# Performance work log

Hardware: AMD Instinct MI355X
Metric: run time of the kernel (lower is better)

The kernel has to match this reference:

```python
import jax, jax.numpy as jnp
import numpy as np

NEG_INF = -9e15
ALPHA = 0.2  # attention leaky_relu slope


def _gat_layer(h, adj_mask, W, a1, a2):
    # h: [N, Fin], W: [Fin, D], a1/a2: [D]
    Wh = h @ W                                   # [N, D]
    f1 = Wh @ a1                                 # [N]
    f2 = Wh @ a2                                 # [N]
    e = jax.nn.leaky_relu(f1[:, None] + f2[None, :], ALPHA)  # [N, N]
    scores = jnp.where(adj_mask, e, NEG_INF)
    att = jax.nn.softmax(scores, axis=-1)        # row-normalized over neighbors
    return att @ Wh                              # [N, D]


def setup_inputs() -> dict:
    key = jax.random.key(0)
    ks = jax.random.split(key, 12)
    N, Fin, H, D, C = 4096, 512, 8, 64, 64
    s = 0.1
    x = jax.random.normal(ks[0], (N, Fin), jnp.float32)
    adj = jax.random.randint(ks[1], (N, N), 0, 2, jnp.int32)
    W = jax.random.normal(ks[2], (H, Fin, D), jnp.float32) * s
    a1 = jax.random.normal(ks[3], (H, D), jnp.float32) * s
    a2 = jax.random.normal(ks[4], (H, D), jnp.float32) * s
    Wo = jax.random.normal(ks[5], (H * D, C), jnp.float32) * s
    ao1 = jax.random.normal(ks[6], (C,), jnp.float32) * s
    ao2 = jax.random.normal(ks[7], (C,), jnp.float32) * s
    W1 = jax.random.normal(ks[8], (512, N), jnp.float32) * 0.01  # nn.Linear(N, 512)
    b1 = jnp.zeros((512,), jnp.float32)
    W2 = jax.random.normal(ks[9], (256, 512), jnp.float32) * 0.04  # nn.Linear(512, 256)
    b2 = jnp.zeros((256,), jnp.float32)
    return {"x": x, "adj": adj, "W": W, "a1": a1, "a2": a2,
            "Wo": Wo, "ao1": ao1, "ao2": ao2,
            "W1": W1, "b1": b1, "W2": W2, "b2": b2}


def reference(x, adj, W, a1, a2, Wo, ao1, ao2, W1, b1, W2, b2):
    mask = adj > 0                                    # [N, N]
    # multi-head dense attention, concat=True -> ELU per head
    heads = jax.vmap(lambda Wk, a1k, a2k: _gat_layer(x, mask, Wk, a1k, a2k))(W, a1, a2)  # [H, N, D]
    h = jax.nn.elu(heads).transpose(1, 0, 2).reshape(x.shape[0], -1)  # [N, H*D]
    # output attention layer, concat=False (no inner ELU), then outer ELU
    out = jax.nn.elu(_gat_layer(h, mask, Wo, ao1, ao2))  # [N, C]
    out = jax.nn.log_softmax(out, axis=0)                # over nodes (dim=0)
    # MLP head on transposed features: [C, N] -> [C, 512] -> [C, 256]
    y = jax.nn.leaky_relu(out.T @ W1.T + b1, 0.1)
    y = y @ W2.T + b2
    return y
```

## Files before the change

### kernel.cpp

```cpp
#include <hip/hip_runtime.h>
#include <hip/hip_bf16.h>
#include <math.h>


#define N_NODES 4096
#define FIN 512
#define NHEAD 8
#define DHEAD 64
#define NCLS 64

typedef unsigned short u16;
typedef unsigned long long u64;
typedef __attribute__((ext_vector_type(8))) short bf16x8;
typedef __attribute__((ext_vector_type(4))) float f32x4;

__device__ __forceinline__ float lrelu02(float x) { return x > 0.f ? x : 0.2f * x; }
__device__ __forceinline__ u16 bf16u(float x) {
    __hip_bfloat16 h = __float2bfloat16(x);
    return __builtin_bit_cast(unsigned short, h);
}
__device__ __forceinline__ f32x4 mfma16(bf16x8 a, bf16x8 b, f32x4 c) {
    return __builtin_amdgcn_mfma_f32_16x16x32_bf16(a, b, c, 0, 0, 0);
}
__device__ __forceinline__ unsigned fkey(float f) {
    unsigned u = __builtin_bit_cast(unsigned, f);
    return (u & 0x80000000u) ? ~u : (u | 0x80000000u);
}
__device__ __forceinline__ float funkey(unsigned k) {
    unsigned u = (k & 0x80000000u) ? (k ^ 0x80000000u) : ~k;
    return __builtin_bit_cast(float, u);
}

__global__ __launch_bounds__(256) void prep(
    const int* __restrict__ adj, u64* __restrict__ mbT, unsigned* __restrict__ gmk,
    const float* __restrict__ x, u16* __restrict__ xB,
    const float* __restrict__ W1, u16* __restrict__ W1B,
    const float* __restrict__ W, const float* __restrict__ Wo,
    u16* __restrict__ WBt, u16* __restrict__ WoBt) {
    __shared__ alignas(16) u16 T[64][72];
    const int bid = blockIdx.x, t = threadIdx.x;
    if (bid < 1024) {
        if (bid == 0 && t < 16) gmk[t] = 0u;
        int nwaves = (1024 * 256) >> 6;
        int wid = (bid * 256 + t) >> 6;
        int lane = t & 63;
        for (int w = wid; w < N_NODES * 64; w += nwaves) {
            int i = w >> 6, wc = w & 63;
            int j = (wc << 6) | lane;
            u64 m = __ballot(adj[(size_t)i * N_NODES + j] > 0);
            if (lane == 0) mbT[(size_t)wc * N_NODES + i] = m;
        }
    } else if (bid < 5120) {
        int i = (bid - 1024) * 256 + t;
        const float* s;
        u16* d;
        if (i < N_NODES * FIN / 4) { s = x; d = xB; }
        else { i -= N_NODES * FIN / 4; s = W1; d = W1B; }
        float4 v = ((const float4*)s)[i];
        ushort4 o = {bf16u(v.x), bf16u(v.y), bf16u(v.z), bf16u(v.w)};
        ((ushort4*)d)[i] = o;
    } else {
        int idx = bid - 5120;
        int y = idx >> 3, xb = idx & 7;
        const float* src = (y < 8) ? W + (size_t)y * FIN * DHEAD : Wo;
        u16* d = (y < 8) ? WBt + (size_t)y * DHEAD * FIN : WoBt;
        const int j0 = xb * 64;
        const int row = t & 63, g = t >> 6;
        #pragma unroll
        for (int k = 0; k < 16; k += 4) {
            float4 v = *(const float4*)(src + (size_t)(j0 + row) * 64 + g * 16 + k);
            T[g * 16 + k + 0][row] = bf16u(v.x);
            T[g * 16 + k + 1][row] = bf16u(v.y);
            T[g * 16 + k + 2][row] = bf16u(v.z);
            T[g * 16 + k + 3][row] = bf16u(v.w);
        }
        __syncthreads();
        const int dd = t >> 2, jc = (t & 3) * 16;
        *(uint4*)(d + (size_t)dd * FIN + j0 + jc) = *(const uint4*)&T[dd][jc];
        *(uint4*)(d + (size_t)dd * FIN + j0 + jc + 8) = *(const uint4*)&T[dd][jc + 8];
    }
}

__global__ __launch_bounds__(256) void gemm_fused(
    const u16* __restrict__ A, int lda, const u16* __restrict__ Bt, int ldb,
    const float* __restrict__ a1a, const float* __restrict__ a2a,
    u16* __restrict__ WhBT, float* __restrict__ f1o, float* __restrict__ f2o,
    unsigned* __restrict__ gmk, int K) {
    __shared__ alignas(16) u16 T[64][72];
    const int t = threadIdx.x, lane = t & 63, wv = t >> 6;
    const int c16 = lane & 15, kg = lane >> 4;
    const int h = blockIdx.x;
    const int bm = blockIdx.y * 64;
    const u16* Ap = A + (size_t)(bm + wv * 16 + c16) * lda + kg * 8;
    const u16* Bp = Bt + (size_t)(h * 64 + c16) * ldb + kg * 8;
    f32x4 acc[4] = {};
    #pragma unroll 4
    for (int k0 = 0; k0 < K; k0 += 32) {
        bf16x8 a = *(const bf16x8*)(Ap + k0);
        #pragma unroll
        for (int ct = 0; ct < 4; ++ct) {
            bf16x8 b = *(const bf16x8*)(Bp + (size_t)ct * 16 * ldb + k0);
            acc[ct] = mfma16(a, b, acc[ct]);
        }
    }
    float a1v[4], a2v[4];
    #pragma unroll
    for (int ct = 0; ct < 4; ++ct) {
        a1v[ct] = a1a[h * 64 + ct * 16 + c16];
        a2v[ct] = a2a[h * 64 + ct * 16 + c16];
    }
    float mx = -1e30f;
    #pragma unroll
    for (int r = 0; r < 4; ++r) {
        float s1 = 0.f, s2 = 0.f;
        int rl = wv * 16 + kg * 4 + r;
        #pragma unroll
        for (int ct = 0; ct < 4; ++ct) {
            float v = acc[ct][r];
            s1 = fmaf(v, a1v[ct], s1);
            s2 = fmaf(v, a2v[ct], s2);
            T[ct * 16 + c16][rl] = bf16u(v);
        }
        #pragma unroll
        for (int off = 1; off < 16; off <<= 1) {
            s1 += __shfl_xor(s1, off, 64);
            s2 += __shfl_xor(s2, off, 64);
        }
        if (c16 == 0) {
            f1o[(size_t)h * N_NODES + bm + rl] = s1;
            f2o[(size_t)h * N_NODES + bm + rl] = s2;
        }
        mx = fmaxf(mx, s2);
    }
    mx = fmaxf(mx, __shfl_xor(mx, 16, 64));
    mx = fmaxf(mx, __shfl_xor(mx, 32, 64));
    if (lane == 0) atomicMax(&gmk[h], fkey(mx));
    __syncthreads();
    const int dd = t >> 2, jc = (t & 3) * 16;
    u16* dst = WhBT + (size_t)(h * 64 + dd) * N_NODES + bm;
    *(uint4*)(dst + jc) = *(const uint4*)&T[dd][jc];
    *(uint4*)(dst + jc + 8) = *(const uint4*)&T[dd][jc + 8];
}

__global__ void coefk(const float* __restrict__ f1, const float* __restrict__ f2,
                      const unsigned* __restrict__ gmk, float2* __restrict__ rowc,
                      float2* __restrict__ uv) {
    int h = blockIdx.y;
    int i = blockIdx.x * 256 + threadIdx.x;
    float g = funkey(gmk[h]);
    float a = f1[(size_t)h * N_NODES + i];
    float s = a + g;
    float M = lrelu02(s);
    rowc[(size_t)h * N_NODES + i] = make_float2(__expf(s - M), __expf(0.2f * s - M));
    float b = f2[(size_t)h * N_NODES + i] - g;
    uv[(size_t)h * N_NODES + i] = make_float2(__expf(b), __expf(0.2f * b));
}

template <int NH, int ROWS, int JSPLIT, int OUTF>
__global__ __launch_bounds__(256) void attn_v5(
    const u16* __restrict__ WhB, const float2* __restrict__ uv,
    const float2* __restrict__ rowc, const u64* __restrict__ mbT,
    float* __restrict__ outp, float* __restrict__ denP) {
    constexpr int NMT = ROWS / 16;
    constexpr int NJT = (N_NODES / 64) / JSPLIT;
    __shared__ alignas(16) u16 pS[2][ROWS][64];
    __shared__ float Tof[(OUTF == 3) ? 64 * (ROWS + 1) : 1];
    const int b = blockIdx.x;
    int h, ib, js;
    if (NH == 8) { h = b & 7; int r = b >> 3; js = r % JSPLIT; ib = r / JSPLIT; }
    else { h = 0; js = b % JSPLIT; ib = b / JSPLIT; }
    const int i0 = ib * ROWS;
    const int jt0 = js * NJT;
    const int t = threadIdx.x, lane = t & 63, wv = t >> 6;
    const int wv_u = __builtin_amdgcn_readfirstlane(wv);

    const float2* __restrict__ uvp = uv + (size_t)h * N_NODES;

    float Aq[16], Bq[16];
    {
        const float2* rcw = rowc + (size_t)h * N_NODES + i0 + wv_u * 16;
        #pragma unroll
        for (int q = 0; q < 16; ++q) {
            float2 rc = rcw[q];
            Aq[q] = __builtin_amdgcn_readfirstlane(rc.x);
            Bq[q] = __builtin_amdgcn_readfirstlane(rc.y);
        }
    }

    const int kg = lane >> 4, c16 = lane & 15;
    const int ocol = wv * 16 + c16;
    const u16* bptr = WhB + ((size_t)h * 64 + ocol) * N_NODES + jt0 * 64 + kg * 8;
    const int sw8 = (c16 & 7) << 3;
    f32x4 acc[NMT] = {};
    f32x4 acc_d[NMT] = {};
    bf16x8 ones;
    #pragma unroll
    for (int i = 0; i < 8; ++i) ones[i] = (short)0x3F80;

    bf16x8 b0 = *(const bf16x8*)(bptr);
    bf16x8 b1 = *(const bf16x8*)(bptr + 32);
    float2 uvv = uvp[jt0 * 64 + lane];
    u64 m[16];
    {
        const u64* mrow = mbT + (size_t)jt0 * N_NODES + i0 + wv_u * 16;
        #pragma unroll
        for (int q = 0; q < 16; ++q) m[q] = mrow[q];
    }

    for (int it = 0; it < NJT; ++it) {
        const int buf = it & 1;
        const int nit = (it + 1 < NJT) ? it + 1 : it;
        bf16x8 nb0 = *(const bf16x8*)(bptr + (size_t)nit * 64);
        bf16x8 nb1 = *(const bf16x8*)(bptr + (size_t)nit * 64 + 32);
        float2 nuv = uvp[(jt0 + nit) * 64 + lane];
        #pragma unroll
        for (int q = 0; q < 16; ++q) {
            unsigned wlo = __builtin_amdgcn_readfirstlane((unsigned)m[q]);
            unsigned whi = __builtin_amdgcn_readfirstlane((unsigned)(m[q] >> 32));
            u64 ws = ((u64)whi << 32) | wlo;
            float tv = fmaxf(Aq[q] * uvv.x, Bq[q] * uvv.y);
            float p;
            asm("v_cndmask_b32 %0, 0, %1, %2" : "=v"(p) : "v"(tv), "s"(ws));
            pS[buf][wv * 16 + q][lane ^ ((q & 7) << 3)] = bf16u(p);
        }
        {
            const u64* mrow = mbT + (size_t)(jt0 + nit) * N_NODES + i0 + wv_u * 16;
            #pragma unroll
            for (int q = 0; q < 16; ++q) m[q] = mrow[q];
        }
        __syncthreads();
        __builtin_amdgcn_s_setprio(1);
        #pragma unroll
        for (int mt = 0; mt < NMT; ++mt) {
            const u16* ap = &pS[buf][mt * 16 + c16][0];
            bf16x8 a0 = *(const bf16x8*)&ap[(kg * 8) ^ sw8];
            bf16x8 a1 = *(const bf16x8*)&ap[(32 + kg * 8) ^ sw8];
            acc[mt] = mfma16(a0, b0, acc[mt]);
            acc[mt] = mfma16(a1, b1, acc[mt]);
            acc_d[mt] = mfma16(a0, ones, acc_d[mt]);
            acc_d[mt] = mfma16(a1, ones, acc_d[mt]);
        }
        __builtin_amdgcn_s_setprio(0);
        b0 = nb0; b1 = nb1; uvv = nuv;
    }

    if constexpr (OUTF == 1) {
        if (wv == 0 && c16 == 0) {
            #pragma unroll
            for (int mt = 0; mt < NMT; ++mt)
                #pragma unroll
                for (int r = 0; r < 4; ++r)
                    denP[(size_t)js * (8 * N_NODES) + (size_t)h * N_NODES +
                         i0 + mt * 16 + kg * 4 + r] = acc_d[mt][r];
        }
        float* dst = outp + (size_t)js * N_NODES * 512;
        #pragma unroll
        for (int mt = 0; mt < NMT; ++mt)
            #pragma unroll
            for (int r = 0; r < 4; ++r)
                dst[(size_t)(i0 + mt * 16 + kg * 4 + r) * 512 + h * 64 + ocol] = acc[mt][r];
    } else {
        if (wv == 0 && c16 == 0) {
            #pragma unroll
            for (int mt = 0; mt < NMT; ++mt)
                #pragma unroll
                for (int r = 0; r < 4; ++r)
                    denP[(size_t)js * N_NODES + i0 + mt * 16 + kg * 4 + r] = acc_d[mt][r];
        }
        #pragma unroll
        for (int mt = 0; mt < NMT; ++mt)
            #pragma unroll
            for (int r = 0; r < 4; ++r)
                Tof[ocol * (ROWS + 1) + mt * 16 + kg * 4 + r] = acc[mt][r];
        __syncthreads();
        const int c = t >> 2, r0 = (t & 3) * 16;
        float* dst = outp + (size_t)js * 64 * N_NODES + (size_t)c * N_NODES + i0 + r0;
        #pragma unroll
        for (int k = 0; k < 16; k += 4) {
            float4 v = {Tof[c * (ROWS + 1) + r0 + k + 0], Tof[c * (ROWS + 1) + r0 + k + 1],
                        Tof[c * (ROWS + 1) + r0 + k + 2], Tof[c * (ROWS + 1) + r0 + k + 3]};
            *(float4*)(dst + k) = v;
        }
    }
}

__global__ __launch_bounds__(256) void combine8(
    const float* __restrict__ part, const float* __restrict__ denp,
    u16* __restrict__ hB) {
    const int t4 = (blockIdx.x * 256 + threadIdx.x) * 4;
    const int i = t4 >> 9, c = t4 & 511, h = c >> 6;
    float4 p0 = *(const float4*)(part + t4);
    float4 p1 = *(const float4*)(part + (size_t)N_NODES * 512 + t4);
    float d = denp[h * N_NODES + i] + denp[8 * N_NODES + h * N_NODES + i];
    float inv = d > 0.f ? 1.f / d : 0.f;
    float v[4] = {(p0.x + p1.x) * inv, (p0.y + p1.y) * inv,
                  (p0.z + p1.z) * inv, (p0.w + p1.w) * inv};
    ushort4 o;
    #pragma unroll
    for (int k = 0; k < 4; ++k) {
        float e = v[k] > 0.f ? v[k] : expm1f(v[k]);
        ((u16*)&o)[k] = bf16u(e);
    }
    *(ushort4*)(hB + t4) = o;
}

__global__ __launch_bounds__(1024) void combine1_lsm(
    const float* __restrict__ partT, const float* __restrict__ denp,
    u16* __restrict__ lsT) {
    __shared__ float vb[N_NODES];
    __shared__ float r[1024];
    const int c = blockIdx.x, t = threadIdx.x;
    const int i = t * 4;
    float4 s = {0.f, 0.f, 0.f, 0.f}, d = {0.f, 0.f, 0.f, 0.f};
    #pragma unroll
    for (int js = 0; js < 8; ++js) {
        float4 pv = *(const float4*)(partT + (size_t)js * 64 * N_NODES +
                                     (size_t)c * N_NODES + i);
        float4 dv = *(const float4*)(denp + (size_t)js * N_NODES + i);
        s.x += pv.x; s.y += pv.y; s.z += pv.z; s.w += pv.w;
        d.x += dv.x; d.y += dv.y; d.z += dv.z; d.w += dv.w;
    }
    float vv[4] = {d.x > 0.f ? s.x / d.x : 0.f, d.y > 0.f ? s.y / d.y : 0.f,
                   d.z > 0.f ? s.z / d.z : 0.f, d.w > 0.f ? s.w / d.w : 0.f};
    float m = -1e30f;
    #pragma unroll
    for (int k = 0; k < 4; ++k) {
        float e = vv[k] > 0.f ? vv[k] : expm1f(vv[k]);
        vb[i + k] = e;
        m = fmaxf(m, e);
    }
    r[t] = m;
    __syncthreads();
    for (int st = 512; st; st >>= 1) {
        if (t < st) r[t] = fmaxf(r[t], r[t + st]);
        __syncthreads();
    }
    m = r[0];
    __syncthreads();
    float sum = 0.f;
    for (int ii = t; ii < N_NODES; ii += 1024) sum += __expf(vb[ii] - m);
    r[t] = sum;
    __syncthreads();
    for (int st = 512; st; st >>= 1) {
        if (t < st) r[t] += r[t + st];
        __syncthreads();
    }
    float lse = m + __logf(r[0]);
    ushort4 o = {bf16u(vb[i] - lse), bf16u(vb[i + 1] - lse),
                 bf16u(vb[i + 2] - lse), bf16u(vb[i + 3] - lse)};
    *(ushort4*)(lsT + (size_t)c * N_NODES + i) = o;
}

__global__ __launch_bounds__(256) void mlp1_mfma(
    const u16* __restrict__ lsT, const u16* __restrict__ W1B,
    float* __restrict__ part) {
    const int t = threadIdx.x, lane = t & 63, wv = t >> 6;
    const int c16 = lane & 15, kg = lane >> 4;
    const int ks = blockIdx.x & 15;
    const int bn = (blockIdx.x >> 4) * 64;
    const int kb = ks * 256;
    const u16* Ap = lsT + (size_t)(wv * 16 + c16) * N_NODES + kb + kg * 8;
    const u16* Bp = W1B + (size_t)(bn + c16) * N_NODES + kb + kg * 8;
    f32x4 acc[4] = {};
    #pragma unroll
    for (int k0 = 0; k0 < 256; k0 += 32) {
        bf16x8 a = *(const bf16x8*)(Ap + k0);
        #pragma unroll
        for (int ct = 0; ct < 4; ++ct) {
            bf16x8 b = *(const bf16x8*)(Bp + (size_t)ct * 16 * N_NODES + k0);
            acc[ct] = mfma16(a, b, acc[ct]);
        }
    }
    float* dst = part + (size_t)ks * 64 * 512;
    #pragma unroll
    for (int ct = 0; ct < 4; ++ct)
        #pragma unroll
        for (int r = 0; r < 4; ++r)
            dst[(size_t)(wv * 16 + kg * 4 + r) * 512 + bn + ct * 16 + c16] = acc[ct][r];
}

__global__ __launch_bounds__(256) void mlp2f(
    const float* __restrict__ part, const float* __restrict__ b1,
    const float* __restrict__ W2, const float* __restrict__ b2,
    float* __restrict__ out) {
    __shared__ alignas(16) float row[512];
    const int c = blockIdx.x, t = threadIdx.x;
    #pragma unroll
    for (int half = 0; half < 2; ++half) {
        int o = t + half * 256;
        float s = 0.f;
        #pragma unroll
        for (int ks = 0; ks < 16; ++ks)
            s += part[(size_t)ks * 32768 + (size_t)c * 512 + o];
        s += b1[o];
        row[o] = s > 0.f ? s : 0.1f * s;
    }
    __syncthreads();
    float acc = 0.f;
    #pragma unroll 4
    for (int o = 0; o < 512; o += 4) {
        float4 w4 = *(const float4*)(W2 + (size_t)t * 512 + o);
        float4 r4 = *(const float4*)(&row[o]);
        acc += w4.x * r4.x + w4.y * r4.y + w4.z * r4.z + w4.w * r4.w;
    }
    out[(size_t)c * 256 + t] = acc + b2[t];
}

extern "C" void kernel_launch(void* const* d_in, const int* in_sizes, int n_in,
                              void* d_out, int out_size, void* d_ws, size_t ws_size,
                              hipStream_t stream) {
    const float* x   = (const float*)d_in[0];
    const int*   adj = (const int*)d_in[1];
    const float* W   = (const float*)d_in[2];
    const float* a1  = (const float*)d_in[3];
    const float* a2  = (const float*)d_in[4];
    const float* Wo  = (const float*)d_in[5];
    const float* ao1 = (const float*)d_in[6];
    const float* ao2 = (const float*)d_in[7];
    const float* W1  = (const float*)d_in[8];
    const float* b1  = (const float*)d_in[9];
    const float* W2  = (const float*)d_in[10];
    const float* b2  = (const float*)d_in[11];
    float* out = (float*)d_out;

    char* ws = (char*)d_ws;
    size_t off = 0;
    auto alloc = [&](size_t bytes) {
        void* p = ws + off;
        off += (bytes + 255) & ~(size_t)255;
        return p;
    };
    u64*     mbT    = (u64*)alloc((size_t)N_NODES * 64 * 8);
    u16*     xB     = (u16*)alloc((size_t)N_NODES * FIN * 2);
    u16*     WBt    = (u16*)alloc((size_t)NHEAD * DHEAD * FIN * 2);
    u16*     WoBt   = (u16*)alloc((size_t)DHEAD * FIN * 2);
    u16*     W1B    = (u16*)alloc((size_t)512 * N_NODES * 2);
    u16*     WhB    = (u16*)alloc((size_t)NHEAD * DHEAD * N_NODES * 2);
    u16*     WhoB   = (u16*)alloc((size_t)DHEAD * N_NODES * 2);
    u16*     hB     = (u16*)alloc((size_t)N_NODES * 512 * 2);
    float*   part8  = (float*)alloc((size_t)2 * N_NODES * 512 * 4);
    float*   den8   = (float*)alloc((size_t)2 * 8 * N_NODES * 4);
    float*   f1b    = (float*)alloc((size_t)9 * N_NODES * 4);
    float*   f2b    = (float*)alloc((size_t)9 * N_NODES * 4);
    unsigned* gmk   = (unsigned*)alloc(16 * 4);
    float2*  rowc   = (float2*)alloc((size_t)9 * N_NODES * 8);
    float2*  uvb    = (float2*)alloc((size_t)9 * N_NODES * 8);
    char*    ov     = (char*)part8;
    float*   partT1 = (float*)(ov);
    float*   den1   = (float*)(ov + ((size_t)8 << 20));
    u16*     lsT    = (u16*)(ov + ((size_t)8 << 20) + (256 << 10));
    float*   part   = (float*)(ov + ((size_t)9 << 20));
    (void)ws_size; (void)in_sizes; (void)n_in; (void)out_size;

    prep<<<5192, 256, 0, stream>>>(adj, mbT, gmk, x, xB, W1, W1B, W, Wo, WBt, WoBt);
    gemm_fused<<<dim3(8, 64), 256, 0, stream>>>(xB, FIN, WBt, FIN, a1, a2,
                                                WhB, f1b, f2b, gmk, FIN);
    coefk<<<dim3(16, 8), 256, 0, stream>>>(f1b, f2b, gmk, rowc, uvb);
    attn_v5<8, 64, 2, 1><<<(N_NODES / 64) * 2 * 8, 256, 0, stream>>>(
        WhB, uvb, rowc, mbT, part8, den8);
    combine8<<<N_NODES * 512 / 4 / 256, 256, 0, stream>>>(part8, den8, hB);
    gemm_fused<<<dim3(1, 64), 256, 0, stream>>>(hB, 512, WoBt, FIN, ao1, ao2,
                                                WhoB, f1b + (size_t)8 * N_NODES,
                                                f2b + (size_t)8 * N_NODES, gmk + 8, FIN);
    coefk<<<dim3(16, 1), 256, 0, stream>>>(f1b + (size_t)8 * N_NODES,
                                           f2b + (size_t)8 * N_NODES, gmk + 8,
                                           rowc + (size_t)8 * N_NODES,
                                           uvb + (size_t)8 * N_NODES);
    attn_v5<1, 64, 8, 3><<<(N_NODES / 64) * 8, 256, 0, stream>>>(
        WhoB, uvb + (size_t)8 * N_NODES, rowc + (size_t)8 * N_NODES, mbT, partT1, den1);
    combine1_lsm<<<64, 1024, 0, stream>>>(partT1, den1, lsT);
    mlp1_mfma<<<128, 256, 0, stream>>>(lsT, W1B, part);
    mlp2f<<<64, 256, 0, stream>>>(part, b1, W2, b2, out);
}
```

Before: 213.5 us.

## Restructure attention to per-wave register P tiles with MFMA-layout adjacency bitmask

Rewrites the attention kernel so each wave builds its probability tile directly in MFMA A-operand register layout, packing with v_cvt_pk_bf16_f32, with no shared-memory staging or block barriers. It also computes the denominator with VALU adds instead of extra MFMAs against a ones vector. The adjacency bitmask is re-laid out in prep to match that per-lane layout, using coalesced int4 loads in place of one strided ballot per row. The output-layer combine and log-softmax are split into a transpose kernel and a row-softmax kernel. The cost is more scalar mask loads per wave, less reuse of WhB across waves, and one more launch.

```diff
diff --git a/kernel.cpp b/kernel.cpp
--- a/kernel.cpp
+++ b/kernel.cpp
@@ -32,26 +32,15 @@
 }
 
 __global__ __launch_bounds__(256) void prep(
-    const int* __restrict__ adj, u64* __restrict__ mbT, unsigned* __restrict__ gmk,
+    const int* __restrict__ adj, u64* __restrict__ mbA, unsigned* __restrict__ gmk,
     const float* __restrict__ x, u16* __restrict__ xB,
     const float* __restrict__ W1, u16* __restrict__ W1B,
     const float* __restrict__ W, const float* __restrict__ Wo,
     u16* __restrict__ WBt, u16* __restrict__ WoBt) {
     __shared__ alignas(16) u16 T[64][72];
     const int bid = blockIdx.x, t = threadIdx.x;
-    if (bid < 1024) {
-        if (bid == 0 && t < 16) gmk[t] = 0u;
-        int nwaves = (1024 * 256) >> 6;
-        int wid = (bid * 256 + t) >> 6;
-        int lane = t & 63;
-        for (int w = wid; w < N_NODES * 64; w += nwaves) {
-            int i = w >> 6, wc = w & 63;
-            int j = (wc << 6) | lane;
-            u64 m = __ballot(adj[(size_t)i * N_NODES + j] > 0);
-            if (lane == 0) mbT[(size_t)wc * N_NODES + i] = m;
-        }
-    } else if (bid < 5120) {
-        int i = (bid - 1024) * 256 + t;
+    if (bid < 4096) {
+        int i = bid * 256 + t;
         const float* s;
         u16* d;
         if (i < N_NODES * FIN / 4) { s = x; d = xB; }
@@ -59,8 +48,30 @@
         float4 v = ((const float4*)s)[i];
         ushort4 o = {bf16u(v.x), bf16u(v.y), bf16u(v.z), bf16u(v.w)};
         ((ushort4*)d)[i] = o;
+    } else if (bid < 8192) {
+        if (bid == 4096 && t < 16) gmk[t] = 0u;
+        const int lane = t & 63;
+        const int task = (bid - 4096) * 4 + (t >> 6);
+        const int g = task >> 6, jt = task & 63;
+        const int r = lane & 15, kq = lane >> 4;
+        const int* ap = adj + (size_t)(g * 16 + r) * N_NODES + jt * 64 + kq * 8;
+        int4 c0 = *(const int4*)(ap);
+        int4 c1 = *(const int4*)(ap + 4);
+        int4 c2 = *(const int4*)(ap + 32);
+        int4 c3 = *(const int4*)(ap + 36);
+        u64 myw = 0;
+        #pragma unroll
+        for (int w = 0; w < 16; ++w) {
+            const int hf = w >> 3, i = w & 7;
+            int val;
+            if (hf == 0) val = (i < 4) ? ((const int*)&c0)[i & 3] : ((const int*)&c1)[i & 3];
+            else         val = (i < 4) ? ((const int*)&c2)[i & 3] : ((const int*)&c3)[i & 3];
+            u64 bal = __ballot(val > 0);
+            if (lane == w) myw = bal;
+        }
+        if (lane < 16) mbA[((size_t)g * 64 + jt) * 16 + lane] = myw;
     } else {
-        int idx = bid - 5120;
+        int idx = bid - 8192;
         int y = idx >> 3, xb = idx & 7;
         const float* src = (y < 8) ? W + (size_t)y * FIN * DHEAD : Wo;
         u16* d = (y < 8) ? WBt + (size_t)y * DHEAD * FIN : WoBt;
@@ -156,132 +167,112 @@
     uv[(size_t)h * N_NODES + i] = make_float2(__expf(b), __expf(0.2f * b));
 }
 
-template <int NH, int ROWS, int JSPLIT, int OUTF>
-__global__ __launch_bounds__(256) void attn_v5(
+template <int NH, int MT, int JSPLIT, int LJS>
+__global__ __launch_bounds__(256) void attn_v6(
     const u16* __restrict__ WhB, const float2* __restrict__ uv,
-    const float2* __restrict__ rowc, const u64* __restrict__ mbT,
+    const float2* __restrict__ rowc, const u64* __restrict__ mbA,
     float* __restrict__ outp, float* __restrict__ denP) {
-    constexpr int NMT = ROWS / 16;
-    constexpr int NJT = (N_NODES / 64) / JSPLIT;
-    __shared__ alignas(16) u16 pS[2][ROWS][64];
-    __shared__ float Tof[(OUTF == 3) ? 64 * (ROWS + 1) : 1];
-    const int b = blockIdx.x;
+    constexpr int NJT = 64 / JSPLIT;
+    constexpr int OC = (NH == 8) ? 512 : 64;
+    const int t = threadIdx.x, lane = t & 63;
+    const int gw = __builtin_amdgcn_readfirstlane(blockIdx.x * 4 + (t >> 6));
     int h, ib, js;
-    if (NH == 8) { h = b & 7; int r = b >> 3; js = r % JSPLIT; ib = r / JSPLIT; }
-    else { h = 0; js = b % JSPLIT; ib = b / JSPLIT; }
-    const int i0 = ib * ROWS;
+    if (NH == 8) { h = gw & 7; int rest = gw >> 3; js = rest & (JSPLIT - 1); ib = rest >> LJS; }
+    else { h = 0; js = gw & (JSPLIT - 1); ib = gw >> LJS; }
+    const int i0 = ib * (MT * 16);
+    const int g0 = i0 >> 4;
     const int jt0 = js * NJT;
-    const int t = threadIdx.x, lane = t & 63, wv = t >> 6;
-    const int wv_u = __builtin_amdgcn_readfirstlane(wv);
-
-    const float2* __restrict__ uvp = uv + (size_t)h * N_NODES;
-
-    float Aq[16], Bq[16];
-    {
-        const float2* rcw = rowc + (size_t)h * N_NODES + i0 + wv_u * 16;
-        #pragma unroll
-        for (int q = 0; q < 16; ++q) {
-            float2 rc = rcw[q];
-            Aq[q] = __builtin_amdgcn_readfirstlane(rc.x);
-            Bq[q] = __builtin_amdgcn_readfirstlane(rc.y);
-        }
-    }
-
     const int kg = lane >> 4, c16 = lane & 15;
-    const int ocol = wv * 16 + c16;
-    const u16* bptr = WhB + ((size_t)h * 64 + ocol) * N_NODES + jt0 * 64 + kg * 8;
-    const int sw8 = (c16 & 7) << 3;
-    f32x4 acc[NMT] = {};
-    f32x4 acc_d[NMT] = {};
-    bf16x8 ones;
-    #pragma unroll
-    for (int i = 0; i < 8; ++i) ones[i] = (short)0x3F80;
-
-    bf16x8 b0 = *(const bf16x8*)(bptr);
-    bf16x8 b1 = *(const bf16x8*)(bptr + 32);
-    float2 uvv = uvp[jt0 * 64 + lane];
-    u64 m[16];
-    {
-        const u64* mrow = mbT + (size_t)jt0 * N_NODES + i0 + wv_u * 16;
-        #pragma unroll
-        for (int q = 0; q < 16; ++q) m[q] = mrow[q];
-    }
+
+    const float* uvf = (const float*)(uv + (size_t)h * N_NODES);
+    const float2* rcp = rowc + (size_t)h * N_NODES;
+
+    float Aq[MT], Bq[MT], den[MT];
+    #pragma unroll
+    for (int mt = 0; mt < MT; ++mt) {
+        float2 rc = rcp[i0 + mt * 16 + c16];
+        Aq[mt] = rc.x; Bq[mt] = rc.y; den[mt] = 0.f;
+    }
+    const u16* bp[4];
+    #pragma unroll
+    for (int ct = 0; ct < 4; ++ct)
+        bp[ct] = WhB + ((size_t)h * 64 + ct * 16 + c16) * N_NODES + kg * 8;
+
+    f32x4 acc[MT][4] = {};
 
     for (int it = 0; it < NJT; ++it) {
-        const int buf = it & 1;
-        const int nit = (it + 1 < NJT) ? it + 1 : it;
-        bf16x8 nb0 = *(const bf16x8*)(bptr + (size_t)nit * 64);
-        bf16x8 nb1 = *(const bf16x8*)(bptr + (size_t)nit * 64 + 32);
-        float2 nuv = uvp[(jt0 + nit) * 64 + lane];
-        #pragma unroll
-        for (int q = 0; q < 16; ++q) {
-            unsigned wlo = __builtin_amdgcn_readfirstlane((unsigned)m[q]);
-            unsigned whi = __builtin_amdgcn_readfirstlane((unsigned)(m[q] >> 32));
-            u64 ws = ((u64)whi << 32) | wlo;
-            float tv = fmaxf(Aq[q] * uvv.x, Bq[q] * uvv.y);
-            float p;
-            asm("v_cndmask_b32 %0, 0, %1, %2" : "=v"(p) : "v"(tv), "s"(ws));
-            pS[buf][wv * 16 + q][lane ^ ((q & 7) << 3)] = bf16u(p);
-        }
-        {
-            const u64* mrow = mbT + (size_t)(jt0 + nit) * N_NODES + i0 + wv_u * 16;
+        const int jt = jt0 + it;
+        const float* up = uvf + (size_t)(jt * 64 + kg * 8) * 2;
+        float4 u0[4], u1[4];
+        #pragma unroll
+        for (int k = 0; k < 4; ++k) {
+            u0[k] = *(const float4*)(up + k * 4);
+            u1[k] = *(const float4*)(up + 64 + k * 4);
+        }
+        bf16x8 bfr[4][2];
+        #pragma unroll
+        for (int ct = 0; ct < 4; ++ct) {
+            bfr[ct][0] = *(const bf16x8*)(bp[ct] + (size_t)jt * 64);
+            bfr[ct][1] = *(const bf16x8*)(bp[ct] + (size_t)jt * 64 + 32);
+        }
+        #pragma unroll
+        for (int mt = 0; mt < MT; ++mt) {
+            const u64* mw = mbA + ((size_t)(g0 + mt) * 64 + jt) * 16;
+            unsigned pk[8];
             #pragma unroll
-            for (int q = 0; q < 16; ++q) m[q] = mrow[q];
-        }
-        __syncthreads();
-        __builtin_amdgcn_s_setprio(1);
-        #pragma unroll
-        for (int mt = 0; mt < NMT; ++mt) {
-            const u16* ap = &pS[buf][mt * 16 + c16][0];
-            bf16x8 a0 = *(const bf16x8*)&ap[(kg * 8) ^ sw8];
-            bf16x8 a1 = *(const bf16x8*)&ap[(32 + kg * 8) ^ sw8];
-            acc[mt] = mfma16(a0, b0, acc[mt]);
-            acc[mt] = mfma16(a1, b1, acc[mt]);
-            acc_d[mt] = mfma16(a0, ones, acc_d[mt]);
-            acc_d[mt] = mfma16(a1, ones, acc_d[mt]);
-        }
-        __builtin_amdgcn_s_setprio(0);
-        b0 = nb0; b1 = nb1; uvv = nuv;
-    }
-
-    if constexpr (OUTF == 1) {
-        if (wv == 0 && c16 == 0) {
+            for (int hf = 0; hf < 2; ++hf) {
+                #pragma unroll
+                for (int k = 0; k < 4; ++k) {
+                    float4 q = hf ? u1[k] : u0[k];
+                    u64 w0 = mw[hf * 8 + 2 * k];
+                    u64 w1 = mw[hf * 8 + 2 * k + 1];
+                    unsigned l0 = __builtin_amdgcn_readfirstlane((unsigned)w0);
+                    unsigned h0 = __builtin_amdgcn_readfirstlane((unsigned)(w0 >> 32));
+                    unsigned l1 = __builtin_amdgcn_readfirstlane((unsigned)w1);
+                    unsigned h1 = __builtin_amdgcn_readfirstlane((unsigned)(w1 >> 32));
+                    u64 ws0 = ((u64)h0 << 32) | l0;
+                    u64 ws1 = ((u64)h1 << 32) | l1;
+                    float t0 = fmaxf(Aq[mt] * q.x, Bq[mt] * q.y);
+                    float t1 = fmaxf(Aq[mt] * q.z, Bq[mt] * q.w);
+                    float p0, p1;
+                    asm("v_cndmask_b32 %0, 0, %1, %2" : "=v"(p0) : "v"(t0), "s"(ws0));
+                    asm("v_cndmask_b32 %0, 0, %1, %2" : "=v"(p1) : "v"(t1), "s"(ws1));
+                    den[mt] += p0 + p1;
+                    unsigned pkd;
+                    asm("v_cvt_pk_bf16_f32 %0, %1, %2" : "=v"(pkd) : "v"(p0), "v"(p1));
+                    pk[hf * 4 + k] = pkd;
+                }
+            }
+            union { unsigned d[4]; bf16x8 v; } ua, ub;
             #pragma unroll
-            for (int mt = 0; mt < NMT; ++mt)
-                #pragma unroll
-                for (int r = 0; r < 4; ++r)
-                    denP[(size_t)js * (8 * N_NODES) + (size_t)h * N_NODES +
-                         i0 + mt * 16 + kg * 4 + r] = acc_d[mt][r];
-        }
-        float* dst = outp + (size_t)js * N_NODES * 512;
-        #pragma unroll
-        for (int mt = 0; mt < NMT; ++mt)
+            for (int k = 0; k < 4; ++k) { ua.d[k] = pk[k]; ub.d[k] = pk[4 + k]; }
+            #pragma unroll
+            for (int ct = 0; ct < 4; ++ct) {
+                acc[mt][ct] = mfma16(ua.v, bfr[ct][0], acc[mt][ct]);
+                acc[mt][ct] = mfma16(ub.v, bfr[ct][1], acc[mt][ct]);
+            }
+        }
+    }
+
+    #pragma unroll
+    for (int mt = 0; mt < MT; ++mt) {
+        den[mt] += __shfl_xor(den[mt], 16, 64);
+        den[mt] += __shfl_xor(den[mt], 32, 64);
+    }
+    float* denDst = (NH == 8) ? denP + (size_t)js * (8 * N_NODES) + (size_t)h * N_NODES
+                              : denP + (size_t)js * N_NODES;
+    if (lane < 16) {
+        #pragma unroll
+        for (int mt = 0; mt < MT; ++mt) denDst[i0 + mt * 16 + lane] = den[mt];
+    }
+    float* dst = outp + (size_t)js * N_NODES * OC + h * 64;
+    #pragma unroll
+    for (int mt = 0; mt < MT; ++mt)
+        #pragma unroll
+        for (int ct = 0; ct < 4; ++ct)
             #pragma unroll
             for (int r = 0; r < 4; ++r)
-                dst[(size_t)(i0 + mt * 16 + kg * 4 + r) * 512 + h * 64 + ocol] = acc[mt][r];
-    } else {
-        if (wv == 0 && c16 == 0) {
-            #pragma unroll
-            for (int mt = 0; mt < NMT; ++mt)
-                #pragma unroll
-                for (int r = 0; r < 4; ++r)
-                    denP[(size_t)js * N_NODES + i0 + mt * 16 + kg * 4 + r] = acc_d[mt][r];
-        }
-        #pragma unroll
-        for (int mt = 0; mt < NMT; ++mt)
-            #pragma unroll
-            for (int r = 0; r < 4; ++r)
-                Tof[ocol * (ROWS + 1) + mt * 16 + kg * 4 + r] = acc[mt][r];
-        __syncthreads();
-        const int c = t >> 2, r0 = (t & 3) * 16;
-        float* dst = outp + (size_t)js * 64 * N_NODES + (size_t)c * N_NODES + i0 + r0;
-        #pragma unroll
-        for (int k = 0; k < 16; k += 4) {
-            float4 v = {Tof[c * (ROWS + 1) + r0 + k + 0], Tof[c * (ROWS + 1) + r0 + k + 1],
-                        Tof[c * (ROWS + 1) + r0 + k + 2], Tof[c * (ROWS + 1) + r0 + k + 3]};
-            *(float4*)(dst + k) = v;
-        }
-    }
+                dst[(size_t)(i0 + mt * 16 + kg * 4 + r) * OC + ct * 16 + c16] = acc[mt][ct][r];
 }
 
 __global__ __launch_bounds__(256) void combine8(
@@ -304,51 +295,77 @@
     *(ushort4*)(hB + t4) = o;
 }
 
-__global__ __launch_bounds__(1024) void combine1_lsm(
-    const float* __restrict__ partT, const float* __restrict__ denp,
-    u16* __restrict__ lsT) {
-    __shared__ float vb[N_NODES];
-    __shared__ float r[1024];
-    const int c = blockIdx.x, t = threadIdx.x;
-    const int i = t * 4;
-    float4 s = {0.f, 0.f, 0.f, 0.f}, d = {0.f, 0.f, 0.f, 0.f};
+__global__ __launch_bounds__(256) void combine1T(
+    const float* __restrict__ part1, const float* __restrict__ den1,
+    float* __restrict__ attoutT) {
+    __shared__ float T[64][65];
+    const int b = blockIdx.x, t = threadIdx.x;
+    const int r0 = b * 64;
+    const int rl = t >> 2, cg = (t & 3) * 16;
+    const int row = r0 + rl;
+    float d = 0.f;
+    #pragma unroll
+    for (int js = 0; js < 8; ++js) d += den1[(size_t)js * N_NODES + row];
+    float inv = d > 0.f ? 1.f / d : 0.f;
+    float s[16] = {};
     #pragma unroll
     for (int js = 0; js < 8; ++js) {
-        float4 pv = *(const float4*)(partT + (size_t)js * 64 * N_NODES +
-                                     (size_t)c * N_NODES + i);
-        float4 dv = *(const float4*)(denp + (size_t)js * N_NODES + i);
-        s.x += pv.x; s.y += pv.y; s.z += pv.z; s.w += pv.w;
-        d.x += dv.x; d.y += dv.y; d.z += dv.z; d.w += dv.w;
-    }
-    float vv[4] = {d.x > 0.f ? s.x / d.x : 0.f, d.y > 0.f ? s.y / d.y : 0.f,
-                   d.z > 0.f ? s.z / d.z : 0.f, d.w > 0.f ? s.w / d.w : 0.f};
+        const float* p = part1 + (size_t)js * N_NODES * 64 + (size_t)row * 64 + cg;
+        #pragma unroll
+        for (int k = 0; k < 16; k += 4) {
+            float4 v = *(const float4*)(p + k);
+            s[k] += v.x; s[k + 1] += v.y; s[k + 2] += v.z; s[k + 3] += v.w;
+        }
+    }
+    #pragma unroll
+    for (int k = 0; k < 16; ++k) {
+        float e = s[k] * inv;
+        T[rl][cg + k] = e > 0.f ? e : expm1f(e);
+    }
+    __syncthreads();
+    const int c = t >> 2, seg = (t & 3) * 16;
+    #pragma unroll
+    for (int k = 0; k < 16; k += 4) {
+        float4 v = {T[seg + k][c], T[seg + k + 1][c], T[seg + k + 2][c], T[seg + k + 3][c]};
+        *(float4*)(attoutT + (size_t)c * N_NODES + r0 + seg + k) = v;
+    }
+}
+
+__global__ __launch_bounds__(256) void lsm_row(const float* __restrict__ aT,
+                                               u16* __restrict__ lsT) {
+    int c = blockIdx.x, t = threadIdx.x;
+    const float* row = aT + (size_t)c * N_NODES;
+    __shared__ float r[256];
     float m = -1e30f;
-    #pragma unroll
-    for (int k = 0; k < 4; ++k) {
-        float e = vv[k] > 0.f ? vv[k] : expm1f(vv[k]);
-        vb[i + k] = e;
-        m = fmaxf(m, e);
+    for (int i = t * 4; i < N_NODES; i += 1024) {
+        float4 v = *(const float4*)(row + i);
+        m = fmaxf(fmaxf(fmaxf(m, v.x), fmaxf(v.y, v.z)), v.w);
     }
     r[t] = m;
     __syncthreads();
-    for (int st = 512; st; st >>= 1) {
-        if (t < st) r[t] = fmaxf(r[t], r[t + st]);
+    for (int s = 128; s; s >>= 1) {
+        if (t < s) r[t] = fmaxf(r[t], r[t + s]);
         __syncthreads();
     }
     m = r[0];
     __syncthreads();
     float sum = 0.f;
-    for (int ii = t; ii < N_NODES; ii += 1024) sum += __expf(vb[ii] - m);
+    for (int i = t * 4; i < N_NODES; i += 1024) {
+        float4 v = *(const float4*)(row + i);
+        sum += __expf(v.x - m) + __expf(v.y - m) + __expf(v.z - m) + __expf(v.w - m);
+    }
     r[t] = sum;
     __syncthreads();
-    for (int st = 512; st; st >>= 1) {
-        if (t < st) r[t] += r[t + st];
+    for (int s = 128; s; s >>= 1) {
+        if (t < s) r[t] += r[t + s];
         __syncthreads();
     }
     float lse = m + __logf(r[0]);
-    ushort4 o = {bf16u(vb[i] - lse), bf16u(vb[i + 1] - lse),
-                 bf16u(vb[i + 2] - lse), bf16u(vb[i + 3] - lse)};
-    *(ushort4*)(lsT + (size_t)c * N_NODES + i) = o;
+    for (int i = t * 4; i < N_NODES; i += 1024) {
+        float4 v = *(const float4*)(row + i);
+        ushort4 o = {bf16u(v.x - lse), bf16u(v.y - lse), bf16u(v.z - lse), bf16u(v.w - lse)};
+        *(ushort4*)(lsT + (size_t)c * N_NODES + i) = o;
+    }
 }
 
 __global__ __launch_bounds__(256) void mlp1_mfma(
@@ -430,7 +447,7 @@
         off += (bytes + 255) & ~(size_t)255;
         return p;
     };
-    u64*     mbT    = (u64*)alloc((size_t)N_NODES * 64 * 8);
+    u64*     mbA    = (u64*)alloc((size_t)256 * 64 * 16 * 8);
     u16*     xB     = (u16*)alloc((size_t)N_NODES * FIN * 2);
     u16*     WBt    = (u16*)alloc((size_t)NHEAD * DHEAD * FIN * 2);
     u16*     WoBt   = (u16*)alloc((size_t)DHEAD * FIN * 2);
@@ -445,19 +462,19 @@
     unsigned* gmk   = (unsigned*)alloc(16 * 4);
     float2*  rowc   = (float2*)alloc((size_t)9 * N_NODES * 8);
     float2*  uvb    = (float2*)alloc((size_t)9 * N_NODES * 8);
-    char*    ov     = (char*)part8;
-    float*   partT1 = (float*)(ov);
-    float*   den1   = (float*)(ov + ((size_t)8 << 20));
-    u16*     lsT    = (u16*)(ov + ((size_t)8 << 20) + (256 << 10));
-    float*   part   = (float*)(ov + ((size_t)9 << 20));
+    char*  ov      = (char*)part8;
+    float* part1   = (float*)(ov);
+    float* den1    = (float*)(ov + ((size_t)8 << 20));
+    float* attoutT = (float*)(ov + ((size_t)9 << 20));
+    u16*   lsT     = (u16*)(ov + ((size_t)10 << 20));
+    float* part    = (float*)(ov + ((size_t)11 << 20));
     (void)ws_size; (void)in_sizes; (void)n_in; (void)out_size;
 
-    prep<<<5192, 256, 0, stream>>>(adj, mbT, gmk, x, xB, W1, W1B, W, Wo, WBt, WoBt);
+    prep<<<8264, 256, 0, stream>>>(adj, mbA, gmk, x, xB, W1, W1B, W, Wo, WBt, WoBt);
     gemm_fused<<<dim3(8, 64), 256, 0, stream>>>(xB, FIN, WBt, FIN, a1, a2,
                                                 WhB, f1b, f2b, gmk, FIN);
     coefk<<<dim3(16, 8), 256, 0, stream>>>(f1b, f2b, gmk, rowc, uvb);
-    attn_v5<8, 64, 2, 1><<<(N_NODES / 64) * 2 * 8, 256, 0, stream>>>(
-        WhB, uvb, rowc, mbT, part8, den8);
+    attn_v6<8, 2, 2, 1><<<512, 256, 0, stream>>>(WhB, uvb, rowc, mbA, part8, den8);
     combine8<<<N_NODES * 512 / 4 / 256, 256, 0, stream>>>(part8, den8, hB);
     gemm_fused<<<dim3(1, 64), 256, 0, stream>>>(hB, 512, WoBt, FIN, ao1, ao2,
                                                 WhoB, f1b + (size_t)8 * N_NODES,
@@ -466,9 +483,10 @@
                                            f2b + (size_t)8 * N_NODES, gmk + 8,
                                            rowc + (size_t)8 * N_NODES,
                                            uvb + (size_t)8 * N_NODES);
-    attn_v5<1, 64, 8, 3><<<(N_NODES / 64) * 8, 256, 0, stream>>>(
-        WhoB, uvb + (size_t)8 * N_NODES, rowc + (size_t)8 * N_NODES, mbT, partT1, den1);
-    combine1_lsm<<<64, 1024, 0, stream>>>(partT1, den1, lsT);
+    attn_v6<1, 1, 8, 3><<<512, 256, 0, stream>>>(
+        WhoB, uvb + (size_t)8 * N_NODES, rowc + (size_t)8 * N_NODES, mbA, part1, den1);
+    combine1T<<<64, 256, 0, stream>>>(part1, den1, attoutT);
+    lsm_row<<<64, 256, 0, stream>>>(attoutT, lsT);
     mlp1_mfma<<<128, 256, 0, stream>>>(lsT, W1B, part);
     mlp2f<<<64, 256, 0, stream>>>(part, b1, W2, b2, out);
 }
```

Result: slower. 239.3 us (+12.1%).
